# Optimization experiments

Measured on AMD Instinct MI355X. Metric: run time of the kernel, lower is better.

Reference implementation:

```python
import jax, jax.numpy as jnp
import numpy as np

# Model dims / constants (from par in init_kwargs)
B, N_IN, NN = 128, 1024, 512
DT, TAU_M, V_TH = 0.05, 10.0, 2.0
ALPHA = 1.0 - DT / TAU_M  # leak factor, 0.995


def setup_inputs() -> dict:
    key = jax.random.key(0)
    k1, k2, k3, k4 = jax.random.split(key, 4)
    x = jax.random.normal(k1, (B, N_IN, NN), dtype=jnp.float32)          # input traces per neuron
    w = jax.random.normal(k2, (N_IN, NN), dtype=jnp.float32) / np.sqrt(N_IN)  # init.normal_(std=1/sqrt(n_in))
    v = jax.random.normal(k3, (B, NN), dtype=jnp.float32)                # membrane potential state
    z = (jax.random.uniform(k4, (B, NN)) < 0.1).astype(jnp.float32)      # previous spikes (0/1)
    return {"x": x, "w": w, "v": v, "z": z}


def reference(x, w, v, z):
    # LIF membrane update, vectorized over the batch (original uses a per-batch Python loop):
    #   v[b] = alpha*v[b] + sum_i x[b,i,:]*w[i,:] - v_th*z[b].detach()
    v_new = ALPHA * v + jnp.sum(x * w[None, :, :], axis=1) - V_TH * jax.lax.stop_gradient(z)
    # threshold nonlinearity -> output spikes
    z_new = (v_new - V_TH > 0).astype(v_new.dtype)
    return v_new, z_new
```

## Files before the change

### kernel.cpp

```cpp
#include <hip/hip_runtime.h>


typedef float f32x4 __attribute__((ext_vector_type(4)));

constexpr int B    = 128;
constexpr int N_IN = 1024;
constexpr int NN   = 512;
constexpr int NN4  = NN / 4;
constexpr float ALPHA = 1.0f - 0.05f / 10.0f;
constexpr float V_TH  = 2.0f;

__global__ __launch_bounds__(256) void lif_partial(
    const f32x4* __restrict__ x4,
    const f32x4* __restrict__ w4,
    f32x4* __restrict__ part)
{
    const int t    = threadIdx.x;
    const int g    = t & 63;
    const int c    = t >> 6;
    const int sub  = blockIdx.x & 15;
    const int bp   = blockIdx.x >> 4;
    const int slab = sub & 1;
    const int ig   = sub >> 1;

    const int b0  = bp * 2;
    const int col = slab * 64 + g;
    const int i0  = ig * 128 + c * 32;

    const f32x4* __restrict__ xp0 =
        x4 + ((size_t)b0 * N_IN + i0) * NN4 + col;
    const f32x4* __restrict__ xp1 = xp0 + (size_t)N_IN * NN4;
    const f32x4* __restrict__ wp  = w4 + (size_t)i0 * NN4 + col;

    f32x4 a0 = {0.f, 0.f, 0.f, 0.f};
    f32x4 a1 = {0.f, 0.f, 0.f, 0.f};
    #pragma unroll 8
    for (int ii = 0; ii < 32; ++ii) {
        f32x4 wv  = wp[(size_t)ii * NN4];
        f32x4 xv0 = __builtin_nontemporal_load(&xp0[(size_t)ii * NN4]);
        f32x4 xv1 = __builtin_nontemporal_load(&xp1[(size_t)ii * NN4]);
        a0 += xv0 * wv;
        a1 += xv1 * wv;
    }

    __shared__ f32x4 red0[256];
    __shared__ f32x4 red1[256];
    red0[t] = a0;
    red1[t] = a1;
    __syncthreads();

    if (t < 128) {
        red0[t] += red0[t + 128];
        red1[t] += red1[t + 128];
    }
    __syncthreads();
    if (t < 64) {
        f32x4 s0 = red0[t] + red0[t + 64];
        f32x4 s1 = red1[t] + red1[t + 64];
        const int cidx = slab * 64 + t;
        part[((size_t)ig * B + b0)     * NN4 + cidx] = s0;
        part[((size_t)ig * B + b0 + 1) * NN4 + cidx] = s1;
    }
}

__global__ __launch_bounds__(256) void lif_finalize(
    const f32x4* __restrict__ part,
    const f32x4* __restrict__ v4,
    const f32x4* __restrict__ z4,
    f32x4* __restrict__ vout4,
    f32x4* __restrict__ zout4)
{
    const int idx = blockIdx.x * 256 + threadIdx.x;
    if (idx >= B * NN4) return;
    f32x4 s = part[idx];
    #pragma unroll
    for (int igr = 1; igr < 8; ++igr)
        s += part[(size_t)igr * B * NN4 + idx];
    f32x4 vv = v4[idx];
    f32x4 zz = z4[idx];
    f32x4 vn = ALPHA * vv + s - V_TH * zz;
    vout4[idx] = vn;
    f32x4 zn;
    zn.x = (vn.x - V_TH > 0.f) ? 1.f : 0.f;
    zn.y = (vn.y - V_TH > 0.f) ? 1.f : 0.f;
    zn.z = (vn.z - V_TH > 0.f) ? 1.f : 0.f;
    zn.w = (vn.w - V_TH > 0.f) ? 1.f : 0.f;
    zout4[idx] = zn;
}

extern "C" void kernel_launch(void* const* d_in, const int* in_sizes, int n_in,
                              void* d_out, int out_size, void* d_ws, size_t ws_size,
                              hipStream_t stream) {
    const f32x4* x = (const f32x4*)d_in[0];
    const f32x4* w = (const f32x4*)d_in[1];
    const f32x4* v = (const f32x4*)d_in[2];
    const f32x4* z = (const f32x4*)d_in[3];
    f32x4* vout = (f32x4*)d_out;
    f32x4* zout = vout + (size_t)B * NN4;
    f32x4* part = (f32x4*)d_ws;

    lif_partial<<<dim3(64 * 16), dim3(256), 0, stream>>>(x, w, part);
    lif_finalize<<<dim3((B * NN4 + 255) / 256), dim3(256), 0, stream>>>(
        part, v, z, vout, zout);
}
```

Measured before the change: 48.84 us.

## Fuse partial reduction and LIF finalize into a single kernel

Each block now reduces over the full input dimension for a 16-column slab and two batch rows, then applies the leak/threshold update directly. This removes the second kernel launch and the workspace round-trip for partial sums. In exchange, each row access is narrower (16 float4 per row segment) and the grid is halved, which may reduce memory coalescing and latency hiding on the bandwidth-bound stream of x.

After: 54.19 us. +10.9%, slower.

```diff
diff --git a/kernel.cpp b/kernel.cpp
--- a/kernel.cpp
+++ b/kernel.cpp
@@ -10,32 +10,32 @@
 constexpr float ALPHA = 1.0f - 0.05f / 10.0f;
 constexpr float V_TH  = 2.0f;
 
-__global__ __launch_bounds__(256) void lif_partial(
+__global__ __launch_bounds__(256) void lif_fused(
     const f32x4* __restrict__ x4,
     const f32x4* __restrict__ w4,
-    f32x4* __restrict__ part)
+    const f32x4* __restrict__ v4,
+    const f32x4* __restrict__ z4,
+    f32x4* __restrict__ vout4,
+    f32x4* __restrict__ zout4)
 {
     const int t    = threadIdx.x;
-    const int g    = t & 63;
-    const int c    = t >> 6;
-    const int sub  = blockIdx.x & 15;
-    const int bp   = blockIdx.x >> 4;
-    const int slab = sub & 1;
-    const int ig   = sub >> 1;
+    const int g    = t & 15;
+    const int c    = t >> 4;
+    const int slab = blockIdx.x & 7;
+    const int bp   = blockIdx.x >> 3;
 
     const int b0  = bp * 2;
-    const int col = slab * 64 + g;
-    const int i0  = ig * 128 + c * 32;
+    const int col = slab * 16 + g;
+    const int i0  = c * 64;
 
-    const f32x4* __restrict__ xp0 =
-        x4 + ((size_t)b0 * N_IN + i0) * NN4 + col;
+    const f32x4* __restrict__ xp0 = x4 + ((size_t)b0 * N_IN + i0) * NN4 + col;
     const f32x4* __restrict__ xp1 = xp0 + (size_t)N_IN * NN4;
     const f32x4* __restrict__ wp  = w4 + (size_t)i0 * NN4 + col;
 
     f32x4 a0 = {0.f, 0.f, 0.f, 0.f};
     f32x4 a1 = {0.f, 0.f, 0.f, 0.f};
     #pragma unroll 8
-    for (int ii = 0; ii < 32; ++ii) {
+    for (int ii = 0; ii < 64; ++ii) {
         f32x4 wv  = wp[(size_t)ii * NN4];
         f32x4 xv0 = __builtin_nontemporal_load(&xp0[(size_t)ii * NN4]);
         f32x4 xv1 = __builtin_nontemporal_load(&xp1[(size_t)ii * NN4]);
@@ -49,43 +49,38 @@
     red1[t] = a1;
     __syncthreads();
 
-    if (t < 128) {
-        red0[t] += red0[t + 128];
-        red1[t] += red1[t + 128];
+    if (t < 128) { red0[t] += red0[t + 128]; red1[t] += red1[t + 128]; }
+    __syncthreads();
+    if (t < 64)  { red0[t] += red0[t + 64];  red1[t] += red1[t + 64];  }
+    __syncthreads();
+    if (t < 32)  { red0[t] += red0[t + 32];  red1[t] += red1[t + 32];  }
+    __syncthreads();
+
+    if (t < 16) {
+        f32x4 s0 = red0[t] + red0[t + 16];
+        f32x4 s1 = red1[t] + red1[t + 16];
+        const int cidx = slab * 16 + t;
+        const int idx0 = b0 * NN4 + cidx;
+        const int idx1 = idx0 + NN4;
+
+        f32x4 vv0 = v4[idx0], zz0 = z4[idx0];
+        f32x4 vv1 = v4[idx1], zz1 = z4[idx1];
+        f32x4 vn0 = ALPHA * vv0 + s0 - V_TH * zz0;
+        f32x4 vn1 = ALPHA * vv1 + s1 - V_TH * zz1;
+        vout4[idx0] = vn0;
+        vout4[idx1] = vn1;
+        f32x4 zn0, zn1;
+        zn0.x = (vn0.x - V_TH > 0.f) ? 1.f : 0.f;
+        zn0.y = (vn0.y - V_TH > 0.f) ? 1.f : 0.f;
+        zn0.z = (vn0.z - V_TH > 0.f) ? 1.f : 0.f;
+        zn0.w = (vn0.w - V_TH > 0.f) ? 1.f : 0.f;
+        zn1.x = (vn1.x - V_TH > 0.f) ? 1.f : 0.f;
+        zn1.y = (vn1.y - V_TH > 0.f) ? 1.f : 0.f;
+        zn1.z = (vn1.z - V_TH > 0.f) ? 1.f : 0.f;
+        zn1.w = (vn1.w - V_TH > 0.f) ? 1.f : 0.f;
+        zout4[idx0] = zn0;
+        zout4[idx1] = zn1;
     }
-    __syncthreads();
-    if (t < 64) {
-        f32x4 s0 = red0[t] + red0[t + 64];
-        f32x4 s1 = red1[t] + red1[t + 64];
-        const int cidx = slab * 64 + t;
-        part[((size_t)ig * B + b0)     * NN4 + cidx] = s0;
-        part[((size_t)ig * B + b0 + 1) * NN4 + cidx] = s1;
-    }
-}
-
-__global__ __launch_bounds__(256) void lif_finalize(
-    const f32x4* __restrict__ part,
-    const f32x4* __restrict__ v4,
-    const f32x4* __restrict__ z4,
-    f32x4* __restrict__ vout4,
-    f32x4* __restrict__ zout4)
-{
-    const int idx = blockIdx.x * 256 + threadIdx.x;
-    if (idx >= B * NN4) return;
-    f32x4 s = part[idx];
-    #pragma unroll
-    for (int igr = 1; igr < 8; ++igr)
-        s += part[(size_t)igr * B * NN4 + idx];
-    f32x4 vv = v4[idx];
-    f32x4 zz = z4[idx];
-    f32x4 vn = ALPHA * vv + s - V_TH * zz;
-    vout4[idx] = vn;
-    f32x4 zn;
-    zn.x = (vn.x - V_TH > 0.f) ? 1.f : 0.f;
-    zn.y = (vn.y - V_TH > 0.f) ? 1.f : 0.f;
-    zn.z = (vn.z - V_TH > 0.f) ? 1.f : 0.f;
-    zn.w = (vn.w - V_TH > 0.f) ? 1.f : 0.f;
-    zout4[idx] = zn;
 }
 
 extern "C" void kernel_launch(void* const* d_in, const int* in_sizes, int n_in,
@@ -97,9 +92,6 @@
     const f32x4* z = (const f32x4*)d_in[3];
     f32x4* vout = (f32x4*)d_out;
     f32x4* zout = vout + (size_t)B * NN4;
-    f32x4* part = (f32x4*)d_ws;
 
-    lif_partial<<<dim3(64 * 16), dim3(256), 0, stream>>>(x, w, part);
-    lif_finalize<<<dim3((B * NN4 + 255) / 256), dim3(256), 0, stream>>>(
-        part, v, z, vout, zout);
+    lif_fused<<<dim3(64 * 8), dim3(256), 0, stream>>>(x, w, v, z, vout, zout);
 }
```
